# Performance work log

Hardware: AMD Instinct MI355X
Metric: run time of the kernel (lower is better)

The kernel has to match this reference:

```python
import jax, jax.numpy as jnp
import numpy as np

# ---- config (matches init_kwargs) ----
D_MODEL = 1024
D_STATE = 16
D_CONV = 4
EXPAND = 2
HEADDIM = 32
NGROUPS = 1
CHUNK = 256
D_INNER = EXPAND * D_MODEL            # 2048
NHEADS = D_INNER // HEADDIM           # 64
D_IN_PROJ = 2 * D_INNER + 2 * NGROUPS * D_STATE + NHEADS  # 4176
CONV_DIM = D_INNER + 2 * NGROUPS * D_STATE                # 2080
BATCH, SEQLEN = 2, 2048
EPS = 1e-5
NEG_INF = -1e9


def setup_inputs() -> dict:
    key = jax.random.key(0)
    ks = jax.random.split(key, 8)
    u = jax.random.normal(ks[0], (BATCH, SEQLEN, D_MODEL), jnp.float32)
    W_in = jax.random.normal(ks[1], (D_IN_PROJ, D_MODEL), jnp.float32) * (1.0 / np.sqrt(D_MODEL))
    conv_w = jax.random.normal(ks[2], (CONV_DIM, 1, D_CONV), jnp.float32) * (1.0 / np.sqrt(D_CONV))
    conv_b = jnp.zeros((CONV_DIM,), jnp.float32)
    dt_bias = jax.random.normal(ks[3], (NHEADS,), jnp.float32) * 0.1
    A_log = jnp.log(1.0 + 15.0 * jax.random.uniform(ks[4], (NHEADS,), jnp.float32))  # A in [1,16]
    D = jnp.ones((NHEADS,), jnp.float32)
    norm_w = jnp.ones((D_INNER,), jnp.float32)
    W_out = jax.random.normal(ks[5], (D_MODEL, D_INNER), jnp.float32) * (1.0 / np.sqrt(D_INNER))
    return dict(u=u, W_in=W_in, conv_w=conv_w, conv_b=conv_b, dt_bias=dt_bias,
                A_log=A_log, D=D, norm_w=norm_w, W_out=W_out)


def _ssd_chunk_scan(x, dt, A, Bm, Cm, Dh):
    """Mamba2 SSD chunked scan.
    x: (b,l,h,p), dt: (b,l,h), A: (h,), Bm/Cm: (b,l,n) [ngroups=1], Dh: (h,).
    """
    b, l, h, p = x.shape
    c = l // CHUNK
    n = Bm.shape[-1]
    xdt = x * dt[..., None]                                  # (b,l,h,p)
    xc = xdt.reshape(b, c, CHUNK, h, p)
    xo = x.reshape(b, c, CHUNK, h, p)
    Bc = Bm.reshape(b, c, CHUNK, n)
    Cc = Cm.reshape(b, c, CHUNK, n)
    Abar = (dt * A).reshape(b, c, CHUNK, h).transpose(0, 3, 1, 2)   # (b,h,c,l)
    Acum = jnp.cumsum(Abar, axis=-1)                                # (b,h,c,l)
    # intra-chunk decay matrix L[i,j] = exp(sum_{j<k<=i} Abar_k), causal
    seg = Acum[..., :, None] - Acum[..., None, :]                   # (b,h,c,l,l)
    causal = jnp.tril(jnp.ones((CHUNK, CHUNK), bool))
    Lmat = jnp.exp(jnp.where(causal, seg, NEG_INF))
    # diagonal (intra-chunk) contribution
    Yd = jnp.einsum('bcln,bcsn,bhcls,bcshp->bclhp', Cc, Bc, Lmat, xc)
    # chunk states
    decay_states = jnp.exp(Acum[..., -1:] - Acum)                   # (b,h,c,l)
    states = jnp.einsum('bcln,bhcl,bclhp->bchpn', Bc, decay_states, xc)
    chunk_decay = jnp.exp(Acum[..., -1])                            # (b,h,c)
    # inter-chunk recurrence over the c axis
    def step(carry, inp):
        s, dec = inp
        new = dec[..., None, None] * carry + s
        return new, carry
    s_t = jnp.moveaxis(states, 1, 0)            # (c,b,h,p,n)
    d_t = jnp.moveaxis(chunk_decay, -1, 0)      # (c,b,h)
    init = jnp.zeros((b, h, p, n), x.dtype)
    _, prev = jax.lax.scan(step, init, (s_t, d_t))
    prev = jnp.moveaxis(prev, 0, 1)             # (b,c,h,p,n) state entering each chunk
    Yo = jnp.einsum('bcln,bchpn,bhcl->bclhp', Cc, prev, jnp.exp(Acum))
    Y = Yd + Yo + xo * Dh[None, None, None, :, None]
    return Y.reshape(b, l, h, p)


def reference(u, W_in, conv_w, conv_b, dt_bias, A_log, D, norm_w, W_out):
    b, l, _ = u.shape
    zxbcdt = u @ W_in.T                                   # (b,l,D_IN_PROJ)
    z = zxbcdt[..., :D_INNER]
    xBC = zxbcdt[..., D_INNER:D_INNER + CONV_DIM]
    dt = jax.nn.softplus(zxbcdt[..., -NHEADS:] + dt_bias)  # (b,l,h)
    # depthwise causal conv1d + SiLU
    xBC_t = xBC.transpose(0, 2, 1)                        # (b, CONV_DIM, l)
    conv = jax.lax.conv_general_dilated(
        xBC_t, conv_w, window_strides=(1,), padding=[(D_CONV - 1, 0)],
        feature_group_count=CONV_DIM)
    xBC = jax.nn.silu(conv + conv_b[None, :, None]).transpose(0, 2, 1)
    x = xBC[..., :D_INNER]
    Bm = xBC[..., D_INNER:D_INNER + NGROUPS * D_STATE]
    Cm = xBC[..., D_INNER + NGROUPS * D_STATE:]
    A = -jnp.exp(A_log)
    Y = _ssd_chunk_scan(x.reshape(b, l, NHEADS, HEADDIM), dt, A, Bm, Cm, D)
    y = Y.reshape(b, l, D_INNER)
    # gated RMSNorm (norm_before_gate=False): normalize(y * silu(z)) * w
    yg = y * jax.nn.silu(z)
    yn = yg * jax.lax.rsqrt(jnp.mean(yg * yg, axis=-1, keepdims=True) + EPS) * norm_w
    out = yn @ W_out.T
    return (out, z)
```

## Files before the change

### kernel.cpp

```cpp
#include <hip/hip_runtime.h>

#define BATCH   2
#define SEQLEN  2048
#define DMODEL  1024
#define DINNER  2048
#define NHEADS  64
#define HEADDIM 32
#define DSTATE  16
#define CONVDIM 2080
#define DINPROJ 4192
#define NPAD    4224
#define CHUNK   256
#define NCHUNK  8
#define BL      (BATCH*SEQLEN)
#define XWIDTH  2144

typedef float          f4    __attribute__((ext_vector_type(4)));
typedef short          s16x8 __attribute__((ext_vector_type(8)));
typedef unsigned short u16x4 __attribute__((ext_vector_type(4)));
typedef __bf16         bf16x8 __attribute__((ext_vector_type(8)));
typedef float          f32x4v __attribute__((ext_vector_type(4)));

#define MFMA16(a,b,c) __builtin_amdgcn_mfma_f32_16x16x32_bf16((a),(b),(c),0,0,0)

__device__ __forceinline__ unsigned short f2bf(float f){
  unsigned int u = __float_as_uint(f);
  u += 0x7FFFu + ((u >> 16) & 1u);
  return (unsigned short)(u >> 16);
}
__device__ __forceinline__ float bf2f(unsigned short u){
  return __uint_as_float(((unsigned int)u) << 16);
}

__device__ __forceinline__ void gload_lds16(const void* g, void* l){
  __builtin_amdgcn_global_load_lds((const __attribute__((address_space(1))) unsigned int*)g,
                                   (__attribute__((address_space(3))) unsigned int*)l,
                                   16, 0, 0);
}

__device__ __forceinline__ bf16x8 f32x8_to_frag(const float* src, bool valid){
  bf16x8 r;
  if (valid) {
    f4 a = *(const f4*)src;
    f4 c = *(const f4*)(src + 4);
    r[0]=(__bf16)a[0]; r[1]=(__bf16)a[1]; r[2]=(__bf16)a[2]; r[3]=(__bf16)a[3];
    r[4]=(__bf16)c[0]; r[5]=(__bf16)c[1]; r[6]=(__bf16)c[2]; r[7]=(__bf16)c[3];
  } else {
    r[0]=(__bf16)0.f; r[1]=(__bf16)0.f; r[2]=(__bf16)0.f; r[3]=(__bf16)0.f;
    r[4]=(__bf16)0.f; r[5]=(__bf16)0.f; r[6]=(__bf16)0.f; r[7]=(__bf16)0.f;
  }
  return r;
}

__device__ __forceinline__ bf16x8 bf16x8_load(const unsigned short* src, bool valid){
  if (valid) {
    s16x8 v = *(const s16x8*)src;
    return *(bf16x8*)&v;
  }
  bf16x8 r;
  r[0]=(__bf16)0.f; r[1]=(__bf16)0.f; r[2]=(__bf16)0.f; r[3]=(__bf16)0.f;
  r[4]=(__bf16)0.f; r[5]=(__bf16)0.f; r[6]=(__bf16)0.f; r[7]=(__bf16)0.f;
  return r;
}

__global__ void cast_f32_bf16(const float* __restrict__ in, unsigned short* __restrict__ out, int n){
  int i = blockIdx.x * 256 + threadIdx.x;
  if (i < n) out[i] = f2bf(in[i]);
}

__global__ void cast_win_pad(const float* __restrict__ in, unsigned short* __restrict__ out){
  int i = blockIdx.x * 256 + threadIdx.x;
  if (i >= NPAD * DMODEL) return;
  int r = i >> 10;
  out[i] = (r < DINPROJ) ? f2bf(in[i]) : (unsigned short)0;
}

template<int MODE>
__global__ __launch_bounds__(256) void gemm_bf16(
    const unsigned short* __restrict__ A,
    const unsigned short* __restrict__ B,
    int K, float* __restrict__ C0, float* __restrict__ C1, int N)
{
  __shared__ unsigned short As[2][128][32];
  __shared__ unsigned short Bs[2][128][32];

  const int nx   = gridDim.x;
  const int flat = blockIdx.y * nx + blockIdx.x;
  const int q    = (nx * gridDim.y) >> 3;
  const int swz  = (flat & 7) * q + (flat >> 3);
  const int bm   = swz / nx, bn = swz % nx;

  const int tid  = threadIdx.x;
  const int wave = tid >> 6, lane = tid & 63;
  const int wm   = (wave >> 1) * 64, wn = (wave & 1) * 64;
  const int lrow = lane & 15, khalf = lane >> 4;
  const int cread = (khalf ^ ((lrow >> 1) & 3)) * 8;

  const int srow = wave * 16 + (lane >> 2);
  const int scol = ((lane & 3) ^ ((lane >> 3) & 3)) * 8;
  const unsigned short* Ag = A + (size_t)(bm * 128 + srow) * K + scol;
  const unsigned short* Bg = B + (size_t)(bn * 128 + srow) * K + scol;
  const int lr0 = wave * 16;

  f32x4v acc[4][4];
  #pragma unroll
  for (int i = 0; i < 4; ++i)
    #pragma unroll
    for (int j = 0; j < 4; ++j)
      acc[i][j] = (f32x4v){0.f,0.f,0.f,0.f};

  auto stage = [&](int buf, int k0){
    gload_lds16(Ag + k0,                   &As[buf][lr0][0]);
    gload_lds16(Ag + k0 + (size_t)64 * K,  &As[buf][64 + lr0][0]);
    gload_lds16(Bg + k0,                   &Bs[buf][lr0][0]);
    gload_lds16(Bg + k0 + (size_t)64 * K,  &Bs[buf][64 + lr0][0]);
  };

  const int NT = K >> 5;
  stage(0, 0);
  stage(1, 32);
  for (int t = 0; t < NT; ++t) {
    const int cur = t & 1;
    if (t + 1 < NT) { asm volatile("s_waitcnt vmcnt(4)" ::: "memory"); }
    else            { asm volatile("s_waitcnt vmcnt(0)" ::: "memory"); }
    __builtin_amdgcn_s_barrier();
    __builtin_amdgcn_sched_barrier(0);
    bf16x8 af[4], bfr[4];
    #pragma unroll
    for (int i = 0; i < 4; ++i) {
      af[i]  = *(const bf16x8*)&As[cur][wm + i * 16 + lrow][cread];
      bfr[i] = *(const bf16x8*)&Bs[cur][wn + i * 16 + lrow][cread];
    }
    __builtin_amdgcn_s_setprio(1);
    #pragma unroll
    for (int mi = 0; mi < 4; ++mi)
      #pragma unroll
      for (int ni = 0; ni < 4; ++ni)
        acc[mi][ni] = MFMA16(af[mi], bfr[ni], acc[mi][ni]);
    __builtin_amdgcn_s_setprio(0);
    __builtin_amdgcn_s_barrier();
    __builtin_amdgcn_sched_barrier(0);
    if (t + 2 < NT) stage(cur, (t + 2) << 5);
  }

  const int orow0 = bm * 128 + wm;
  const int ocol0 = bn * 128 + wn;
  #pragma unroll
  for (int mi = 0; mi < 4; ++mi)
    #pragma unroll
    for (int ni = 0; ni < 4; ++ni) {
      int col  = ocol0 + ni * 16 + lrow;
      int rowb = orow0 + mi * 16 + khalf * 4;
      #pragma unroll
      for (int r = 0; r < 4; ++r) {
        int row = rowb + r;
        float v = acc[mi][ni][r];
        if (MODE == 0) {
          if (col < DINNER)        C0[(size_t)row * DINNER + col] = v;
          else if (col < DINPROJ)  C1[(size_t)row * XWIDTH + (col - DINNER)] = v;
        } else {
          C0[(size_t)row * N + col] = v;
        }
      }
    }
}

__global__ void conv_dt_kernel(const float* __restrict__ xbcdt,
                               const float* __restrict__ conv_w, const float* __restrict__ conv_b,
                               const float* __restrict__ dt_bias,
                               unsigned short* __restrict__ xconv, float* __restrict__ dtout)
{
  int idx = blockIdx.x * 256 + threadIdx.x;
  if (idx >= BL * XWIDTH) return;
  int ch = idx % XWIDTH;
  int bl = idx / XWIDTH;
  int l  = bl & (SEQLEN - 1);
  if (ch < CONVDIM) {
    float acc = conv_b[ch];
    #pragma unroll
    for (int j = 0; j < 4; ++j) {
      int ls = l - 3 + j;
      float x = (ls >= 0) ? xbcdt[(size_t)(bl - 3 + j) * XWIDTH + ch] : 0.f;
      acc += conv_w[ch * 4 + j] * x;
    }
    float s = acc / (1.f + __expf(-acc));
    xconv[(size_t)bl * CONVDIM + ch] = f2bf(s);
  } else {
    int h = ch - CONVDIM;
    float x = xbcdt[(size_t)bl * XWIDTH + ch] + dt_bias[h];
    float dtv = (x > 20.f) ? x : log1pf(__expf(x));
    dtout[bl * NHEADS + h] = dtv;
  }
}

__global__ __launch_bounds__(256) void ssd_phaseA(
    const unsigned short* __restrict__ xconv, const float* __restrict__ dt,
    const float* __restrict__ A_log,
    float* __restrict__ acum, float* __restrict__ decay, float* __restrict__ states)
{
  int bc = blockIdx.x, h = blockIdx.y;
  int b = bc >> 3;
  int t = threadIdx.x;
  __shared__ float sAc[256], sCoef[256], sDt[256];
  __shared__ float sB[256][16];
  __shared__ float sX[256][32];
  int rowbase = b * SEQLEN + (bc & 7) * CHUNK;
  float dtv = dt[(rowbase + t) * NHEADS + h];
  float Av  = -__expf(A_log[h]);
  sAc[t] = dtv * Av; sDt[t] = dtv;
  for (int i = t; i < 256 * 16; i += 256) { int l = i >> 4, n = i & 15; sB[l][n] = bf2f(xconv[(size_t)(rowbase + l) * CONVDIM + DINNER + n]); }
  for (int i = t; i < 256 * 32; i += 256) { int l = i >> 5, p = i & 31; sX[l][p] = bf2f(xconv[(size_t)(rowbase + l) * CONVDIM + h * 32 + p]); }
  __syncthreads();
  for (int off = 1; off < 256; off <<= 1) {
    float add = (t >= off) ? sAc[t - off] : 0.f;
    __syncthreads();
    sAc[t] += add;
    __syncthreads();
  }
  int bch = bc * 64 + h;
  acum[(size_t)bch * 256 + t] = sAc[t];
  float last = sAc[255];
  if (t == 0) decay[bch] = __expf(last);
  sCoef[t] = sDt[t] * __expf(last - sAc[t]);
  __syncthreads();
  #pragma unroll
  for (int o = 0; o < 2; ++o) {
    int oi = t + o * 256;
    int p = oi >> 4, n = oi & 15;
    float acc = 0.f;
    for (int l = 0; l < 256; ++l) acc += sCoef[l] * sB[l][n] * sX[l][p];
    states[(size_t)bch * 512 + oi] = acc;
  }
}

__global__ void ssd_phaseB(const float* __restrict__ states, const float* __restrict__ decay,
                           float* __restrict__ prev)
{
  int bh = blockIdx.x;
  int b = bh >> 6, h = bh & 63;
  int t = threadIdx.x;
  float carry = 0.f;
  for (int c = 0; c < NCHUNK; ++c) {
    int bch = (b * 8 + c) * 64 + h;
    size_t base = (size_t)bch * 512 + t;
    prev[base] = carry;
    carry = decay[bch] * carry + states[base];
  }
}

__global__ __launch_bounds__(256, 2) void ssd_phaseC_mfma(
    const unsigned short* __restrict__ xconv, const float* __restrict__ dt,
    const float* __restrict__ acum, const float* __restrict__ prev,
    const float* __restrict__ Dvec, float* __restrict__ y)
{
  const int bc = blockIdx.x, h = blockIdx.y;
  const int b = bc >> 3;
  const int rowbase = b * SEQLEN + (bc & 7) * CHUNK;
  const int bch = bc * 64 + h;
  const int tid = threadIdx.x, wave = tid >> 6, lane = tid & 63;
  const int l16 = lane & 15, khalf = lane >> 4;

  __shared__ float sAcum[256];
  __shared__ __bf16 sXT[32][264];
  __shared__ __bf16 sP[4][2][16][40];

  if (tid < 256) sAcum[tid] = acum[(size_t)bch * 256 + tid];
  {
    int l  = tid >> 3;
    int p0 = (tid & 7) * 4;
    #pragma unroll
    for (int pass = 0; pass < 8; ++pass) {
      int ls = l + pass * 32;
      const unsigned short* xr = xconv + (size_t)(rowbase + ls) * CONVDIM + h * 32 + p0;
      u16x4 v = *(const u16x4*)xr;
      float dtl = dt[(rowbase + ls) * NHEADS + h];
      #pragma unroll
      for (int j = 0; j < 4; ++j) sXT[p0 + j][ls] = (__bf16)(bf2f(v[j]) * dtl);
    }
  }

  const bool kv = (khalf < 2);
  bf16x8 bfr[16], cfr[4], pvf[2];
  #pragma unroll
  for (int i = 0; i < 16; ++i)
    bfr[i] = bf16x8_load(xconv + (size_t)(rowbase + i * 16 + l16) * CONVDIM + DINNER + khalf * 8, kv);
  #pragma unroll
  for (int t = 0; t < 4; ++t)
    cfr[t] = bf16x8_load(xconv + (size_t)(rowbase + (wave + 4 * t) * 16 + l16) * CONVDIM + DINNER + DSTATE + khalf * 8, kv);
  #pragma unroll
  for (int pt = 0; pt < 2; ++pt)
    pvf[pt] = f32x8_to_frag(prev + (size_t)bch * 512 + (pt * 16 + l16) * 16 + khalf * 8, kv);
  __syncthreads();

  const float Dh = Dvec[h];
  #pragma unroll
  for (int t = 0; t < 4; ++t) {
    const int LT = wave + 4 * t;
    const int lbase = LT * 16;
    float al[4], el[4];
    #pragma unroll
    for (int r = 0; r < 4; ++r) { al[r] = sAcum[lbase + khalf * 4 + r]; el[r] = __expf(al[r]); }
    f32x4v y0 = MFMA16(cfr[t], pvf[0], ((f32x4v){0.f,0.f,0.f,0.f}));
    f32x4v y1 = MFMA16(cfr[t], pvf[1], ((f32x4v){0.f,0.f,0.f,0.f}));
    #pragma unroll
    for (int r = 0; r < 4; ++r) { y0[r] *= el[r]; y1[r] *= el[r]; }

    #pragma unroll
    for (int kp = 0; kp < 8; ++kp) {
      if (2 * kp <= LT) {
        f32x4v s0 = MFMA16(cfr[t], bfr[2 * kp],     ((f32x4v){0.f,0.f,0.f,0.f}));
        f32x4v s1 = MFMA16(cfr[t], bfr[2 * kp + 1], ((f32x4v){0.f,0.f,0.f,0.f}));
        const int buf = kp & 1;
        #pragma unroll
        for (int r = 0; r < 4; ++r) {
          int l  = lbase + khalf * 4 + r;
          int sA = 2 * kp * 16 + l16;
          int sB2 = sA + 16;
          float p0 = (sA  <= l) ? s0[r] * __expf(al[r] - sAcum[sA])  : 0.f;
          float p1 = (sB2 <= l) ? s1[r] * __expf(al[r] - sAcum[sB2]) : 0.f;
          sP[wave][buf][khalf * 4 + r][l16]      = (__bf16)p0;
          sP[wave][buf][khalf * 4 + r][16 + l16] = (__bf16)p1;
        }
        bf16x8 pa  = *(const bf16x8*)&sP[wave][buf][l16][khalf * 8];
        bf16x8 xf0 = *(const bf16x8*)&sXT[l16][kp * 32 + khalf * 8];
        bf16x8 xf1 = *(const bf16x8*)&sXT[16 + l16][kp * 32 + khalf * 8];
        y0 = MFMA16(pa, xf0, y0);
        y1 = MFMA16(pa, xf1, y1);
      }
    }

    #pragma unroll
    for (int r = 0; r < 4; ++r) {
      int lg = rowbase + lbase + khalf * 4 + r;
      const unsigned short* xr = xconv + (size_t)lg * CONVDIM + h * 32;
      float* yr = y + (size_t)lg * DINNER + h * 32;
      yr[l16]      = y0[r] + Dh * bf2f(xr[l16]);
      yr[16 + l16] = y1[r] + Dh * bf2f(xr[16 + l16]);
    }
  }
}

__global__ __launch_bounds__(256) void gate_norm(const float* __restrict__ y,
    const float* __restrict__ z, const float* __restrict__ norm_w,
    unsigned short* __restrict__ ynbf)
{
  int row = blockIdx.x, t = threadIdx.x;
  const float* yr = y + (size_t)row * DINNER;
  const float* zr = z + (size_t)row * DINNER;
  float vals[8];
  float ss = 0.f;
  #pragma unroll
  for (int i = 0; i < 8; ++i) {
    int ci = t + i * 256;
    float zv = zr[ci];
    float g = zv / (1.f + __expf(-zv));
    float v = yr[ci] * g;
    vals[i] = v; ss += v * v;
  }
  #pragma unroll
  for (int o = 1; o < 64; o <<= 1) ss += __shfl_xor(ss, o);
  __shared__ float sred[4];
  if ((t & 63) == 0) sred[t >> 6] = ss;
  __syncthreads();
  float tot = sred[0] + sred[1] + sred[2] + sred[3];
  float scale = rsqrtf(tot * (1.f / DINNER) + 1e-5f);
  #pragma unroll
  for (int i = 0; i < 8; ++i) {
    int ci = t + i * 256;
    ynbf[(size_t)row * DINNER + ci] = f2bf(vals[i] * scale * norm_w[ci]);
  }
}

extern "C" void kernel_launch(void* const* d_in, const int* in_sizes, int n_in,
                              void* d_out, int out_size, void* d_ws, size_t ws_size,
                              hipStream_t stream)
{
  const float* u       = (const float*)d_in[0];
  const float* W_in    = (const float*)d_in[1];
  const float* conv_w  = (const float*)d_in[2];
  const float* conv_b  = (const float*)d_in[3];
  const float* dt_bias = (const float*)d_in[4];
  const float* A_log   = (const float*)d_in[5];
  const float* Dv      = (const float*)d_in[6];
  const float* norm_w  = (const float*)d_in[7];
  const float* W_out   = (const float*)d_in[8];

  float* out  = (float*)d_out;
  float* zout = out + (size_t)BL * DMODEL;

  char* ws = (char*)d_ws;
  size_t off = 0;
  auto alloc = [&](size_t bytes){ size_t o = off; off += (bytes + 255) & ~(size_t)255; return o; };
  size_t o_ubf    = alloc((size_t)BL * DMODEL * 2);
  size_t o_wbf    = alloc((size_t)NPAD * DMODEL * 2);
  size_t o_xbcdt  = alloc((size_t)BL * XWIDTH * 4);
  size_t o_xconv  = alloc((size_t)BL * CONVDIM * 2);
  size_t o_dt     = alloc((size_t)BL * NHEADS * 4);
  size_t o_acum   = alloc((size_t)1024 * 256 * 4);
  size_t o_decay  = alloc((size_t)1024 * 4);
  size_t o_states = alloc((size_t)1024 * 512 * 4);
  size_t o_prev   = alloc((size_t)1024 * 512 * 4);
  size_t o_ynbf   = alloc((size_t)BL * DINNER * 2);

  unsigned short* ubf    = (unsigned short*)(ws + o_ubf);
  unsigned short* wbf    = (unsigned short*)(ws + o_wbf);
  float*          xbcdt  = (float*)(ws + o_xbcdt);
  unsigned short* xconv  = (unsigned short*)(ws + o_xconv);
  float*          dtws   = (float*)(ws + o_dt);
  float*          acum   = (float*)(ws + o_acum);
  float*          decay  = (float*)(ws + o_decay);
  float*          states = (float*)(ws + o_states);
  float*          prevb  = (float*)(ws + o_prev);
  unsigned short* ynbf   = (unsigned short*)(ws + o_ynbf);
  unsigned short* woutbf = ubf;
  float*          ywork  = xbcdt;

  cast_f32_bf16<<<(BL * DMODEL) / 256, 256, 0, stream>>>(u, ubf, BL * DMODEL);
  cast_win_pad<<<(NPAD * DMODEL) / 256, 256, 0, stream>>>(W_in, wbf);

  gemm_bf16<0><<<dim3(NPAD / 128, BL / 128), 256, 0, stream>>>(ubf, wbf, DMODEL, zout, xbcdt, 0);

  conv_dt_kernel<<<(BL * XWIDTH) / 256, 256, 0, stream>>>(xbcdt, conv_w, conv_b, dt_bias, xconv, dtws);

  ssd_phaseA<<<dim3(16, 64), 256, 0, stream>>>(xconv, dtws, A_log, acum, decay, states);
  ssd_phaseB<<<128, 512, 0, stream>>>(states, decay, prevb);
  ssd_phaseC_mfma<<<dim3(16, 64), 256, 0, stream>>>(xconv, dtws, acum, prevb, Dv, ywork);

  gate_norm<<<BL, 256, 0, stream>>>(ywork, zout, norm_w, ynbf);

  cast_f32_bf16<<<(DMODEL * DINNER) / 256, 256, 0, stream>>>(W_out, woutbf, DMODEL * DINNER);

  gemm_bf16<1><<<dim3(DMODEL / 128, BL / 128), 256, 0, stream>>>(ynbf, woutbf, DINNER, out, nullptr, DMODEL);
}
```

Baseline: 225.7 us.

## Use 256x256-tile 8-wave GEMM with BK=64 for input projection

Replaces the 128x128-tile in-projection GEMM with a dedicated 512-thread kernel using 256x256 output tiles, K-step 64, and interleaved staging of the next tile between MFMA groups. Larger tiles raise arithmetic intensity and cut global/L2 traffic per FLOP. The cost is padding N to 4352, which adds wasted columns. The grid also shrinks to 17x16=272 blocks, with possible wave-quantization and occupancy effects from the large LDS and register footprint.

```diff
diff --git a/kernel.cpp b/kernel.cpp
--- a/kernel.cpp
+++ b/kernel.cpp
@@ -9,7 +9,7 @@
 #define DSTATE  16
 #define CONVDIM 2080
 #define DINPROJ 4192
-#define NPAD    4224
+#define NPAD    4352
 #define CHUNK   256
 #define NCHUNK  8
 #define BL      (BATCH*SEQLEN)
@@ -75,11 +75,115 @@
   out[i] = (r < DINPROJ) ? f2bf(in[i]) : (unsigned short)0;
 }
 
-template<int MODE>
-__global__ __launch_bounds__(256) void gemm_bf16(
+__global__ __launch_bounds__(512) void gemm256_in(
     const unsigned short* __restrict__ A,
     const unsigned short* __restrict__ B,
-    int K, float* __restrict__ C0, float* __restrict__ C1, int N)
+    float* __restrict__ C0, float* __restrict__ C1)
+{
+  __shared__ unsigned short As[2][2][128][64];
+  __shared__ unsigned short Bs[2][2][128][64];
+  const int K = DMODEL;
+
+  const int nx   = gridDim.x;
+  const int flat = blockIdx.y * nx + blockIdx.x;
+  const int q    = (nx * gridDim.y) >> 3;
+  const int swz  = (flat & 7) * q + (flat >> 3);
+  const int bm   = swz / nx, bn = swz % nx;
+
+  const int tid  = threadIdx.x;
+  const int wave = tid >> 6, lane = tid & 63;
+  const int wr   = wave >> 2, wc = wave & 3;
+  const int l16  = lane & 15, khalf = lane >> 4;
+
+  const int srow8  = lane >> 3;
+  const int schunk = (lane & 7) ^ srow8;
+  const unsigned short* Asrc = A + (size_t)(bm * 256 + wave * 8 + srow8) * K + schunk * 8;
+  const unsigned short* Bsrc = B + (size_t)(bn * 256 + wave * 8 + srow8) * K + schunk * 8;
+
+  auto stageHalf = [&](int buf, int kind, int k0){
+    const unsigned short* s = (kind < 2) ? (Asrc + (size_t)(kind & 1) * 128 * K + k0)
+                                         : (Bsrc + (size_t)(kind & 1) * 128 * K + k0);
+    unsigned short* d = (kind < 2) ? &As[buf][kind & 1][wave * 8][0]
+                                   : &Bs[buf][kind & 1][wave * 8][0];
+    gload_lds16(s, d);
+    gload_lds16(s + (size_t)64 * K, d + 4096);
+  };
+
+#define AFRAG(i,ks) (*(const bf16x8*)&As[cur][wr][(i)*16 + l16][((((ks)*4 + khalf)) ^ (l16 & 7)) * 8])
+#define BFRAG(n,ks) (*(const bf16x8*)&Bs[cur][wc >> 1][(wc & 1)*64 + (n)*16 + l16][((((ks)*4 + khalf)) ^ (l16 & 7)) * 8])
+
+  f32x4v acc[8][4];
+  #pragma unroll
+  for (int i = 0; i < 8; ++i)
+    #pragma unroll
+    for (int j = 0; j < 4; ++j)
+      acc[i][j] = (f32x4v){0.f,0.f,0.f,0.f};
+
+  stageHalf(0, 0, 0); stageHalf(0, 1, 0); stageHalf(0, 2, 0); stageHalf(0, 3, 0);
+  asm volatile("s_waitcnt vmcnt(0)" ::: "memory");
+  __builtin_amdgcn_s_barrier();
+  __builtin_amdgcn_sched_barrier(0);
+
+  const int NT = K >> 6;
+  for (int t = 0; t < NT; ++t) {
+    const int cur = t & 1, nxt = cur ^ 1;
+    const int k1 = (t + 1) << 6;
+    bf16x8 bfm[4][2];
+    #pragma unroll
+    for (int p = 0; p < 4; ++p) {
+      bf16x8 a00 = AFRAG(2*p,   0), a01 = AFRAG(2*p,   1);
+      bf16x8 a10 = AFRAG(2*p+1, 0), a11 = AFRAG(2*p+1, 1);
+      if (p == 0) {
+        #pragma unroll
+        for (int n = 0; n < 4; ++n) { bfm[n][0] = BFRAG(n,0); bfm[n][1] = BFRAG(n,1); }
+      }
+      if (t + 1 < NT) stageHalf(nxt, p, k1);
+      asm volatile("s_waitcnt lgkmcnt(0)" ::: "memory");
+      __builtin_amdgcn_sched_barrier(0);
+      __builtin_amdgcn_s_barrier();
+      __builtin_amdgcn_sched_barrier(0);
+      __builtin_amdgcn_s_setprio(1);
+      #pragma unroll
+      for (int n = 0; n < 4; ++n) {
+        acc[2*p][n]   = MFMA16(a00, bfm[n][0], acc[2*p][n]);
+        acc[2*p][n]   = MFMA16(a01, bfm[n][1], acc[2*p][n]);
+        acc[2*p+1][n] = MFMA16(a10, bfm[n][0], acc[2*p+1][n]);
+        acc[2*p+1][n] = MFMA16(a11, bfm[n][1], acc[2*p+1][n]);
+      }
+      __builtin_amdgcn_s_setprio(0);
+      __builtin_amdgcn_sched_barrier(0);
+    }
+    if (t + 1 < NT) {
+      asm volatile("s_waitcnt vmcnt(0)" ::: "memory");
+      __builtin_amdgcn_s_barrier();
+      __builtin_amdgcn_sched_barrier(0);
+    }
+  }
+#undef AFRAG
+#undef BFRAG
+
+  const int orow0 = bm * 256 + wr * 128;
+  const int ocol0 = bn * 256 + wc * 64;
+  #pragma unroll
+  for (int mi = 0; mi < 8; ++mi)
+    #pragma unroll
+    for (int ni = 0; ni < 4; ++ni) {
+      int col  = ocol0 + ni * 16 + l16;
+      int rowb = orow0 + mi * 16 + khalf * 4;
+      #pragma unroll
+      for (int r = 0; r < 4; ++r) {
+        float v = acc[mi][ni][r];
+        int row = rowb + r;
+        if (col < DINNER)        C0[(size_t)row * DINNER + col] = v;
+        else if (col < DINPROJ)  C1[(size_t)row * XWIDTH + (col - DINNER)] = v;
+      }
+    }
+}
+
+__global__ __launch_bounds__(256) void gemm_bf16_out(
+    const unsigned short* __restrict__ A,
+    const unsigned short* __restrict__ B,
+    int K, float* __restrict__ C0, int N)
 {
   __shared__ unsigned short As[2][128][32];
   __shared__ unsigned short Bs[2][128][32];
@@ -152,16 +256,8 @@
       int col  = ocol0 + ni * 16 + lrow;
       int rowb = orow0 + mi * 16 + khalf * 4;
       #pragma unroll
-      for (int r = 0; r < 4; ++r) {
-        int row = rowb + r;
-        float v = acc[mi][ni][r];
-        if (MODE == 0) {
-          if (col < DINNER)        C0[(size_t)row * DINNER + col] = v;
-          else if (col < DINPROJ)  C1[(size_t)row * XWIDTH + (col - DINNER)] = v;
-        } else {
-          C0[(size_t)row * N + col] = v;
-        }
-      }
+      for (int r = 0; r < 4; ++r)
+        C0[(size_t)(rowb + r) * N + col] = acc[mi][ni][r];
     }
 }
 
@@ -418,7 +514,7 @@
   cast_f32_bf16<<<(BL * DMODEL) / 256, 256, 0, stream>>>(u, ubf, BL * DMODEL);
   cast_win_pad<<<(NPAD * DMODEL) / 256, 256, 0, stream>>>(W_in, wbf);
 
-  gemm_bf16<0><<<dim3(NPAD / 128, BL / 128), 256, 0, stream>>>(ubf, wbf, DMODEL, zout, xbcdt, 0);
+  gemm256_in<<<dim3(NPAD / 256, BL / 256), 512, 0, stream>>>(ubf, wbf, zout, xbcdt);
 
   conv_dt_kernel<<<(BL * XWIDTH) / 256, 256, 0, stream>>>(xbcdt, conv_w, conv_b, dt_bias, xconv, dtws);
 
@@ -430,5 +526,5 @@
 
   cast_f32_bf16<<<(DMODEL * DINNER) / 256, 256, 0, stream>>>(W_out, woutbf, DMODEL * DINNER);
 
-  gemm_bf16<1><<<dim3(DMODEL / 128, BL / 128), 256, 0, stream>>>(ynbf, woutbf, DINNER, out, nullptr, DMODEL);
-}
+  gemm_bf16_out<<<dim3(DMODEL / 128, BL / 128), 256, 0, stream>>>(ynbf, woutbf, DINNER, out, DMODEL);
+}
```

Measured after the change: 233.0 us. +3.2%, slower.
